# Performance work log

Measured on AMD Instinct MI355X. Metric: run time of the kernel, lower is better.

Reference implementation:

```python
import jax, jax.numpy as jnp
import numpy as np

N_IDX = 4
N_LATENT = 6
D_IDX = 2 ** N_IDX
D_LATENT = 2 ** N_LATENT
D = D_IDX * D_LATENT  # 1024
TIME_EMBED = 128
BATCH = 32


def _build_H():
    # S_plus |k> = |(k+1) mod d_idx>, H_idx = S_plus + S_plus^T, H = H_idx kron I_latent
    S_plus = np.zeros((D_IDX, D_IDX), dtype=np.float32)
    for k in range(D_IDX):
        S_plus[(k + 1) % D_IDX, k] = 1.0
    H_idx = S_plus + S_plus.T
    H = np.kron(H_idx, np.eye(D_LATENT, dtype=np.float32))
    return jnp.asarray(H)


def setup_inputs() -> dict:
    key = jax.random.key(0)
    k_rho, k_t, k_w1, k_b1, k_w2, k_b2 = jax.random.split(key, 6)
    # PSD density-like rho so the trace normalization is well-conditioned
    A = jax.random.normal(k_rho, (BATCH, D, D), dtype=jnp.float32)
    rho = jnp.einsum('bij,bkj->bik', A, A) / D
    t = jax.random.uniform(k_t, (BATCH,), dtype=jnp.float32)
    # lambda_net: Linear(1, E) -> SiLU -> Linear(E, 1) -> Tanh (torch Linear: weight (out,in))
    w1 = jax.random.normal(k_w1, (TIME_EMBED, 1), dtype=jnp.float32) * 1.0
    b1 = jax.random.uniform(k_b1, (TIME_EMBED,), dtype=jnp.float32, minval=-1.0, maxval=1.0)
    w2 = jax.random.normal(k_w2, (1, TIME_EMBED), dtype=jnp.float32) * (1.0 / np.sqrt(TIME_EMBED))
    b2 = jax.random.uniform(k_b2, (1,), dtype=jnp.float32, minval=-0.09, maxval=0.09)
    H = _build_H()
    return {'rho': rho, 't': t, 'w1': w1, 'b1': b1, 'w2': w2, 'b2': b2, 'H': H}


def reference(rho, t, w1, b1, w2, b2, H):
    # lambda(t) = 0.1 * tanh(Linear(SiLU(Linear(t))))
    x = t[:, None]  # (B, 1)
    h = jax.nn.silu(x @ w1.T + b1)  # (B, E)
    lam = jnp.tanh(h @ w2.T + b2)[:, 0] * 0.1  # (B,)
    # Shared eigendecomposition of constant symmetric H
    eigvals, eigvecs = jnp.linalg.eigh(H)  # (D,), (D, D)
    exp_diag = jnp.exp(-lam[:, None] * eigvals[None, :])  # (B, D)
    # U_b = V diag(exp_diag_b) V^T, batched
    U = jnp.einsum('id,bd,jd->bij', eigvecs, exp_diag, eigvecs)  # (B, D, D)
    rho_out = jnp.einsum('bij,bjk,blk->bil', U, rho, U)  # U rho U^T
    trace = jnp.trace(rho_out, axis1=-2, axis2=-1)[:, None, None]
    return rho_out / jnp.maximum(trace, 1e-8)
```

## Files before the change

### kernel.cpp

```cpp
#include <hip/hip_runtime.h>
#include <stdint.h>

#define DI 16
#define DD 1024
#define NB 32
#define PI8  0.39269908169872414f

#define AS1 __attribute__((address_space(1)))
#define AS3 __attribute__((address_space(3)))

#define WS_E   0
#define WS_TRP (NB*256)

__global__ __launch_bounds__(256)
void k_trace(const float* __restrict__ rho,
             const float* __restrict__ t,
             const float* __restrict__ w1,
             const float* __restrict__ b1,
             const float* __restrict__ w2,
             const float* __restrict__ b2,
             float* __restrict__ ws) {
    int g = blockIdx.x;
    int b = blockIdx.y;
    int tid = threadIdx.x;
    __shared__ float lam_sh;
    __shared__ float ck[16];
    __shared__ float Gs[16];
    __shared__ float part[4];

    if (tid < 64) {
        float tb = t[b];
        float z0 = tb * w1[tid]      + b1[tid];
        float z1 = tb * w1[tid + 64] + b1[tid + 64];
        float h0 = z0 / (1.0f + expf(-z0));
        float h1 = z1 / (1.0f + expf(-z1));
        float v = h0 * w2[tid] + h1 * w2[tid + 64];
        #pragma unroll
        for (int off = 32; off; off >>= 1) v += __shfl_down(v, off, 64);
        if (tid == 0) lam_sh = tanhf(v + b2[0]) * 0.1f;
    }
    if (tid >= 64 && tid < 80) ck[tid - 64] = cosf(PI8 * (float)(tid - 64));
    __syncthreads();
    float lam = lam_sh;

    if (g == 0) {
        int i = tid >> 4, j = tid & 15, r = (i - j) & 15;
        float se = 0.0f;
        #pragma unroll
        for (int k = 0; k < 16; k++)
            se += expf(-2.0f * lam * ck[k]) * ck[(k * r) & 15];
        ws[WS_E + b * 256 + tid] = se * 0.0625f;
    }

    int c = g >> 2;
    if (tid < 16) {
        int r = (c - tid) & 15;
        float sg = 0.0f;
        #pragma unroll
        for (int k = 0; k < 16; k++)
            sg += expf(-4.0f * lam * ck[k]) * ck[(k * r) & 15];
        Gs[tid] = sg * 0.0625f;
    }
    __syncthreads();

    const float* base = rho + (size_t)b * DD * DD + (size_t)(g * 16) * DD;
    int d   = tid >> 4;
    int sel = tid & 15;
    float gd = Gs[d];
    float s = 0.0f;
    #pragma unroll
    for (int it = 0; it < 16; it++) {
        int p = (g * 16 + it) & 63;
        float4 v = *(const float4*)(base + (size_t)it * DD + tid * 4);
        if ((p >> 2) == sel) {
            int e = p & 3;
            s += gd * (e == 0 ? v.x : e == 1 ? v.y : e == 2 ? v.z : v.w);
        }
    }
    #pragma unroll
    for (int off = 32; off; off >>= 1) s += __shfl_down(s, off, 64);
    if ((tid & 63) == 0) part[tid >> 6] = s;
    __syncthreads();
    if (tid == 0)
        ws[WS_TRP + b * 64 + g] = part[0] + part[1] + part[2] + part[3];
}

__global__ __launch_bounds__(256, 2)
void k_main(const float* __restrict__ rho,
            const float* __restrict__ ws,
            float* __restrict__ out) {
    __shared__ __align__(16) float S[16 * 512];
    __shared__ float T[16 * 516];
    __shared__ float Es[256];
    __shared__ float sinv_sh;

    int qt  = blockIdx.x;
    int p   = blockIdx.y;
    int b   = blockIdx.z;
    int tid = threadIdx.x;
    int q0  = qt * 32;

    if (tid < 64) {
        ((float4*)Es)[tid] = ((const float4*)(ws + WS_E + b * 256))[tid];
        float v = ws[WS_TRP + b * 64 + tid];
        #pragma unroll
        for (int off = 32; off; off >>= 1) v += __shfl_down(v, off, 64);
        if (tid == 0) sinv_sh = 1.0f / fmaxf(v, 1e-8f);
    }

    const float* rbase = rho + (size_t)b * (DD * DD) + q0;
    #pragma unroll
    for (int it = 0; it < 8; it++) {
        int g  = it * 256 + tid;
        int c  = g >> 7;
        int r  = g & 127;
        int d  = r >> 3;
        int q4 = r & 7;
        const float* ga = rbase + (size_t)(c * 64 + p) * DD + d * 64 + q4 * 4;
        int gw = it * 256 + (tid & ~63);
        unsigned fo = (unsigned)((gw >> 7) * 512 + (gw & 127) * 4);
        __builtin_amdgcn_global_load_lds((const AS1 uint32_t*)ga,
                                         (AS3 uint32_t*)&S[fo], 16, 0, 0);
    }

    asm volatile("s_waitcnt vmcnt(4) lgkmcnt(0)\n\ts_barrier" ::: "memory");
    __builtin_amdgcn_sched_barrier(0);

    int ah = tid >> 7;
    int d  = (tid >> 3) & 15;
    int qq = (tid & 7) * 4;
    {
        float4 acc[8];
        #pragma unroll
        for (int i = 0; i < 8; i++) acc[i] = make_float4(0.f, 0.f, 0.f, 0.f);

        #pragma unroll
        for (int c = 0; c < 8; c++) {
            float4 s4 = *(float4*)&S[c * 512 + d * 32 + qq];
            float4 e0 = *(float4*)&Es[c * 16 + ah * 8];
            float4 e1 = *(float4*)&Es[c * 16 + ah * 8 + 4];
            acc[0].x += e0.x * s4.x; acc[0].y += e0.x * s4.y; acc[0].z += e0.x * s4.z; acc[0].w += e0.x * s4.w;
            acc[1].x += e0.y * s4.x; acc[1].y += e0.y * s4.y; acc[1].z += e0.y * s4.z; acc[1].w += e0.y * s4.w;
            acc[2].x += e0.z * s4.x; acc[2].y += e0.z * s4.y; acc[2].z += e0.z * s4.z; acc[2].w += e0.z * s4.w;
            acc[3].x += e0.w * s4.x; acc[3].y += e0.w * s4.y; acc[3].z += e0.w * s4.z; acc[3].w += e0.w * s4.w;
            acc[4].x += e1.x * s4.x; acc[4].y += e1.x * s4.y; acc[4].z += e1.x * s4.z; acc[4].w += e1.x * s4.w;
            acc[5].x += e1.y * s4.x; acc[5].y += e1.y * s4.y; acc[5].z += e1.y * s4.z; acc[5].w += e1.y * s4.w;
            acc[6].x += e1.z * s4.x; acc[6].y += e1.z * s4.y; acc[6].z += e1.z * s4.z; acc[6].w += e1.z * s4.w;
            acc[7].x += e1.w * s4.x; acc[7].y += e1.w * s4.y; acc[7].z += e1.w * s4.z; acc[7].w += e1.w * s4.w;
        }

        asm volatile("s_waitcnt vmcnt(0)\n\ts_barrier" ::: "memory");
        __builtin_amdgcn_sched_barrier(0);

        #pragma unroll
        for (int c = 8; c < 16; c++) {
            float4 s4 = *(float4*)&S[c * 512 + d * 32 + qq];
            float4 e0 = *(float4*)&Es[c * 16 + ah * 8];
            float4 e1 = *(float4*)&Es[c * 16 + ah * 8 + 4];
            acc[0].x += e0.x * s4.x; acc[0].y += e0.x * s4.y; acc[0].z += e0.x * s4.z; acc[0].w += e0.x * s4.w;
            acc[1].x += e0.y * s4.x; acc[1].y += e0.y * s4.y; acc[1].z += e0.y * s4.z; acc[1].w += e0.y * s4.w;
            acc[2].x += e0.z * s4.x; acc[2].y += e0.z * s4.y; acc[2].z += e0.z * s4.z; acc[2].w += e0.z * s4.w;
            acc[3].x += e0.w * s4.x; acc[3].y += e0.w * s4.y; acc[3].z += e0.w * s4.z; acc[3].w += e0.w * s4.w;
            acc[4].x += e1.x * s4.x; acc[4].y += e1.x * s4.y; acc[4].z += e1.x * s4.z; acc[4].w += e1.x * s4.w;
            acc[5].x += e1.y * s4.x; acc[5].y += e1.y * s4.y; acc[5].z += e1.y * s4.z; acc[5].w += e1.y * s4.w;
            acc[6].x += e1.z * s4.x; acc[6].y += e1.z * s4.y; acc[6].z += e1.z * s4.z; acc[6].w += e1.z * s4.w;
            acc[7].x += e1.w * s4.x; acc[7].y += e1.w * s4.y; acc[7].z += e1.w * s4.z; acc[7].w += e1.w * s4.w;
        }

        #pragma unroll
        for (int ai = 0; ai < 8; ai++)
            *(float4*)&T[(ah * 8 + ai) * 516 + d * 32 + qq] = acc[ai];
    }
    __syncthreads();

    {
        int bp = (tid >> 3) & 15;
        float Eb[16];
        #pragma unroll
        for (int j4 = 0; j4 < 4; j4++) {
            float4 e = *(float4*)&Es[bp * 16 + j4 * 4];
            Eb[4 * j4 + 0] = e.x; Eb[4 * j4 + 1] = e.y; Eb[4 * j4 + 2] = e.z; Eb[4 * j4 + 3] = e.w;
        }
        float sinv = sinv_sh;
        float* obase = out + (size_t)b * (DD * DD) + (size_t)p * DD + bp * 64 + q0 + qq;
        #pragma unroll
        for (int ai = 0; ai < 8; ai++) {
            int a = ah * 8 + ai;
            float4 acc = make_float4(0.f, 0.f, 0.f, 0.f);
            #pragma unroll
            for (int dd = 0; dd < 16; dd++) {
                float4 t4 = *(float4*)&T[a * 516 + dd * 32 + qq];
                acc.x += Eb[dd] * t4.x; acc.y += Eb[dd] * t4.y;
                acc.z += Eb[dd] * t4.z; acc.w += Eb[dd] * t4.w;
            }
            acc.x *= sinv; acc.y *= sinv; acc.z *= sinv; acc.w *= sinv;
            *(float4*)(obase + (size_t)a * (64 * DD)) = acc;
        }
    }
}

extern "C" void kernel_launch(void* const* d_in, const int* in_sizes, int n_in,
                              void* d_out, int out_size, void* d_ws, size_t ws_size,
                              hipStream_t stream) {
    const float* rho = (const float*)d_in[0];
    const float* t   = (const float*)d_in[1];
    const float* w1  = (const float*)d_in[2];
    const float* b1  = (const float*)d_in[3];
    const float* w2  = (const float*)d_in[4];
    const float* b2  = (const float*)d_in[5];
    float* out = (float*)d_out;
    float* ws  = (float*)d_ws;

    k_trace<<<dim3(64, NB), 256, 0, stream>>>(rho, t, w1, b1, w2, b2, ws);
    k_main <<<dim3(2, 64, NB), 256, 0, stream>>>(rho, ws, out);
}
```

Measured before the change: 71.59 us.

## Compute trace from only needed diagonal elements and alias T onto S LDS buffer

```diff
diff --git a/kernel.cpp b/kernel.cpp
--- a/kernel.cpp
+++ b/kernel.cpp
@@ -20,12 +20,12 @@
              const float* __restrict__ w2,
              const float* __restrict__ b2,
              float* __restrict__ ws) {
-    int g = blockIdx.x;
+    int x = blockIdx.x;
     int b = blockIdx.y;
     int tid = threadIdx.x;
     __shared__ float lam_sh;
     __shared__ float ck[16];
-    __shared__ float Gs[16];
+    __shared__ float gam[16];
     __shared__ float part[4];
 
     if (tid < 64) {
@@ -43,7 +43,7 @@
     __syncthreads();
     float lam = lam_sh;
 
-    if (g == 0) {
+    if (x == 0) {
         int i = tid >> 4, j = tid & 15, r = (i - j) & 15;
         float se = 0.0f;
         #pragma unroll
@@ -52,29 +52,28 @@
         ws[WS_E + b * 256 + tid] = se * 0.0625f;
     }
 
-    int c = g >> 2;
     if (tid < 16) {
-        int r = (c - tid) & 15;
         float sg = 0.0f;
         #pragma unroll
         for (int k = 0; k < 16; k++)
-            sg += expf(-4.0f * lam * ck[k]) * ck[(k * r) & 15];
-        Gs[tid] = sg * 0.0625f;
-    }
-    __syncthreads();
-
-    const float* base = rho + (size_t)b * DD * DD + (size_t)(g * 16) * DD;
-    int d   = tid >> 4;
-    int sel = tid & 15;
-    float gd = Gs[d];
+            sg += expf(-4.0f * lam * ck[k]) * ck[(k * tid) & 15];
+        gam[tid] = sg * 0.0625f;
+    }
+    __syncthreads();
+
+    const float* bbase = rho + (size_t)b * DD * DD;
+    int nA = 16 - x;
     float s = 0.0f;
     #pragma unroll
-    for (int it = 0; it < 16; it++) {
-        int p = (g * 16 + it) & 63;
-        float4 v = *(const float4*)(base + (size_t)it * DD + tid * 4);
-        if ((p >> 2) == sel) {
-            int e = p & 3;
-            s += gd * (e == 0 ? v.x : e == 1 ? v.y : e == 2 ? v.z : v.w);
+    for (int it = 0; it < 5; it++) {
+        int idx = it * 256 + tid;
+        if (idx < 17 * 64) {
+            int pr = idx >> 6, p = idx & 63;
+            int c  = (pr < nA) ? x : 15 - x;
+            int d  = (pr < nA) ? x + pr : (15 - x) + (pr - nA);
+            int r  = d - c;
+            float w = gam[r] * (r ? 2.0f : 1.0f);
+            s += w * bbase[(size_t)(c * 64 + p) * DD + d * 64 + p];
         }
     }
     #pragma unroll
@@ -82,7 +81,7 @@
     if ((tid & 63) == 0) part[tid >> 6] = s;
     __syncthreads();
     if (tid == 0)
-        ws[WS_TRP + b * 64 + g] = part[0] + part[1] + part[2] + part[3];
+        ws[WS_TRP + b * 8 + x] = part[0] + part[1] + part[2] + part[3];
 }
 
 __global__ __launch_bounds__(256, 2)
@@ -90,7 +89,6 @@
             const float* __restrict__ ws,
             float* __restrict__ out) {
     __shared__ __align__(16) float S[16 * 512];
-    __shared__ float T[16 * 516];
     __shared__ float Es[256];
     __shared__ float sinv_sh;
 
@@ -102,7 +100,7 @@
 
     if (tid < 64) {
         ((float4*)Es)[tid] = ((const float4*)(ws + WS_E + b * 256))[tid];
-        float v = ws[WS_TRP + b * 64 + tid];
+        float v = (tid < 8) ? ws[WS_TRP + b * 8 + tid] : 0.0f;
         #pragma unroll
         for (int off = 32; off; off >>= 1) v += __shfl_down(v, off, 64);
         if (tid == 0) sinv_sh = 1.0f / fmaxf(v, 1e-8f);
@@ -167,9 +165,10 @@
             acc[7].x += e1.w * s4.x; acc[7].y += e1.w * s4.y; acc[7].z += e1.w * s4.z; acc[7].w += e1.w * s4.w;
         }
 
+        __syncthreads();
         #pragma unroll
         for (int ai = 0; ai < 8; ai++)
-            *(float4*)&T[(ah * 8 + ai) * 516 + d * 32 + qq] = acc[ai];
+            *(float4*)&S[(ah * 8 + ai) * 512 + d * 32 + qq] = acc[ai];
     }
     __syncthreads();
 
@@ -189,7 +188,7 @@
             float4 acc = make_float4(0.f, 0.f, 0.f, 0.f);
             #pragma unroll
             for (int dd = 0; dd < 16; dd++) {
-                float4 t4 = *(float4*)&T[a * 516 + dd * 32 + qq];
+                float4 t4 = *(float4*)&S[a * 512 + dd * 32 + qq];
                 acc.x += Eb[dd] * t4.x; acc.y += Eb[dd] * t4.y;
                 acc.z += Eb[dd] * t4.z; acc.w += Eb[dd] * t4.w;
             }
@@ -211,6 +210,6 @@
     float* out = (float*)d_out;
     float* ws  = (float*)d_ws;
 
-    k_trace<<<dim3(64, NB), 256, 0, stream>>>(rho, t, w1, b1, w2, b2, ws);
+    k_trace<<<dim3(8, NB), 256, 0, stream>>>(rho, t, w1, b1, w2, b2, ws);
     k_main <<<dim3(2, 64, NB), 256, 0, stream>>>(rho, ws, out);
 }
```

Result: faster. 64.26 us (-10.2%).
